# Kernel optimization log

Measured on AMD Instinct MI355X. Metric: run time of the kernel, lower is better.

The kernel has to match this reference:

```python
import jax, jax.numpy as jnp
import numpy as np

# Fixed genome topology (layered DAG, topologically ordered levels)
B = 4096      # batch
N_IN = 512    # input nodes
H1 = 1536     # hidden level 1
H2 = 1536     # hidden level 2
N_OUT = 512   # output nodes
FAN = 32      # fan-in per non-input node


def setup_inputs() -> dict:
    key = jax.random.key(0)
    ks = jax.random.split(key, 10)
    x = jax.random.normal(ks[0], (B, N_IN), dtype=jnp.float32)
    # level 1: sources among inputs [0, N_IN)
    src0 = jax.random.randint(ks[1], (H1 * FAN,), 0, N_IN, dtype=jnp.int32)
    dst0 = jax.random.randint(ks[2], (H1 * FAN,), 0, H1, dtype=jnp.int32)
    w0 = jax.random.normal(ks[3], (H1 * FAN,), dtype=jnp.float32) * 0.1
    # level 2: sources among inputs + level1 [0, N_IN+H1)
    src1 = jax.random.randint(ks[4], (H2 * FAN,), 0, N_IN + H1, dtype=jnp.int32)
    dst1 = jax.random.randint(ks[5], (H2 * FAN,), 0, H2, dtype=jnp.int32)
    w1 = jax.random.normal(ks[6], (H2 * FAN,), dtype=jnp.float32) * 0.1
    # output level: sources among all earlier nodes [0, N_IN+H1+H2)
    src2 = jax.random.randint(ks[7], (N_OUT * FAN,), 0, N_IN + H1 + H2, dtype=jnp.int32)
    dst2 = jax.random.randint(ks[8], (N_OUT * FAN,), 0, N_OUT, dtype=jnp.int32)
    w2 = jax.random.normal(ks[9], (N_OUT * FAN,), dtype=jnp.float32) * 0.1
    return dict(x=x, src0=src0, dst0=dst0, w0=w0,
                src1=src1, dst1=dst1, w1=w1,
                src2=src2, dst2=dst2, w2=w2)


def _level(node_values, src, dst, w, size):
    # per-edge weighted gather: [B, E]
    vals = node_values[:, src] * w
    # scatter-add into destination nodes of this level: [B, size]
    agg = jnp.zeros((node_values.shape[0], size), node_values.dtype).at[:, dst].add(vals)
    # per-node activation (genome.activation == 'relu'); relu(0)=0 matches
    # original's behavior of leaving unconnected nodes at zero
    return jax.nn.relu(agg)


def reference(x, src0, dst0, w0, src1, dst1, w1, src2, dst2, w2):
    nv = x                                        # [B, N_IN]
    h1 = _level(nv, src0, dst0, w0, H1)           # [B, H1]
    nv = jnp.concatenate([nv, h1], axis=1)        # [B, N_IN+H1]
    h2 = _level(nv, src1, dst1, w1, H2)           # [B, H2]
    nv = jnp.concatenate([nv, h2], axis=1)        # [B, N_IN+H1+H2]
    out = _level(nv, src2, dst2, w2, N_OUT)       # [B, N_OUT]
    return out
```

## Files before the change

kernel.cpp:

```cpp
#include <hip/hip_runtime.h>
#include <hip/hip_fp16.h>
#include <stdint.h>

#define BATCH 4096
#define N_IN  512
#define H1    1536
#define H2    1536
#define N_OUT 512
#define FAN   32
#define E0 (H1 * FAN)
#define E1 (H2 * FAN)
#define E2 (N_OUT * FAN)
#define ETOT (E0 + E1 + E2)
#define K1 N_IN
#define K2 (N_IN + H1)
#define K3 (N_IN + H1 + H2)

#define NVSTRIDE 3648
#define NVBYTES  ((size_t)BATCH * NVSTRIDE * 2)
#define W0BYTES  ((size_t)H1 * K1 * 2)
#define W1BYTES  ((size_t)H2 * K2 * 2)
#define W2BYTES  ((size_t)N_OUT * K3 * 2)

typedef _Float16 f16x8 __attribute__((ext_vector_type(8)));
typedef float    f32x4 __attribute__((ext_vector_type(4)));

__global__ __launch_bounds__(256) void k_xcvt(const float* __restrict__ x,
                                              __half* __restrict__ nvT) {
    const int t  = blockIdx.x * 256 + threadIdx.x;
    const int n  = t >> 6;
    const int c8 = t & 63;
    const float4 f0 = *(const float4*)(x + (size_t)n * N_IN + c8 * 8);
    const float4 f1 = *(const float4*)(x + (size_t)n * N_IN + c8 * 8 + 4);
    const __half2 a = __floats2half2_rn(f0.x, f0.y);
    const __half2 b = __floats2half2_rn(f0.z, f0.w);
    const __half2 c = __floats2half2_rn(f1.x, f1.y);
    const __half2 d = __floats2half2_rn(f1.z, f1.w);
    uint4 u;
    u.x = *(const uint32_t*)&a; u.y = *(const uint32_t*)&b;
    u.z = *(const uint32_t*)&c; u.w = *(const uint32_t*)&d;
    *(uint4*)(nvT + (size_t)n * NVSTRIDE + c8 * 8) = u;
}

__device__ __forceinline__ void atomic_add_half(__half* addr, float val) {
    uint32_t* base = (uint32_t*)((size_t)addr & ~(size_t)3);
    const bool hi  = ((size_t)addr & 2) != 0;
    uint32_t old = *base, assumed;
    do {
        assumed = old;
        __half2 h2 = *(__half2*)&assumed;
        float f = (hi ? __high2float(h2) : __low2float(h2)) + val;
        __half2 nh = hi ? __halves2half2(__low2half(h2), __float2half_rn(f))
                        : __halves2half2(__float2half_rn(f), __high2half(h2));
        old = atomicCAS(base, assumed, *(uint32_t*)&nh);
    } while (old != assumed);
}

__global__ __launch_bounds__(256) void k_wfill(const int* __restrict__ src,
                                               const int* __restrict__ dst,
                                               const float* __restrict__ w,
                                               __half* __restrict__ Wd, const int K) {
    const int e = blockIdx.x * 256 + threadIdx.x;
    atomic_add_half(Wd + (size_t)dst[e] * K + src[e], w[e]);
}

__global__ __launch_bounds__(256) void k_wfill_all(
        const int* __restrict__ s0, const int* __restrict__ d0, const float* __restrict__ w0,
        const int* __restrict__ s1, const int* __restrict__ d1, const float* __restrict__ w1,
        const int* __restrict__ s2, const int* __restrict__ d2, const float* __restrict__ w2,
        __half* __restrict__ W0d, __half* __restrict__ W1d, __half* __restrict__ W2d) {
    const int e = blockIdx.x * 256 + threadIdx.x;
    if (e < E0)            atomic_add_half(W0d + (size_t)d0[e] * K1 + s0[e], w0[e]);
    else if (e < E0 + E1) { const int i = e - E0;      atomic_add_half(W1d + (size_t)d1[i] * K2 + s1[i], w1[i]); }
    else                  { const int i = e - E0 - E1; atomic_add_half(W2d + (size_t)d2[i] * K3 + s2[i], w2[i]); }
}

template<int BM, bool F32OUT>
__global__ __launch_bounds__(256, 2)
void k_gemm(const __half* __restrict__ A,
            const __half* __restrict__ Bt,
            __half* __restrict__ Ch,
            float* __restrict__ Cf,
            const int K) {
    constexpr int FM = BM / 32;
    constexpr int WR = BM / 2;
    __shared__ __half lA[2][BM * 64];
    __shared__ __half lB[2][128 * 64];
    const int tid  = threadIdx.x;
    const int lane = tid & 63;
    const int wv   = tid >> 6;
    const int wr   = wv >> 1, wc = wv & 1;
    const int m0   = blockIdx.y * BM;
    const int n0   = blockIdx.x * 128;
    const int lrow = lane >> 3;
    const int lchk = lane & 7;

    f32x4 acc[FM][4] = {};

#define STAGE(BUF, KT) {                                                         \
    _Pragma("unroll")                                                            \
    for (int it = 0; it < BM / 32; ++it) {                                       \
        const int row = it * 32 + wv * 8 + lrow;                                 \
        const int sc  = lchk ^ (row & 7);                                        \
        __builtin_amdgcn_global_load_lds(                                        \
            (const __attribute__((address_space(1))) void*)(const void*)         \
                (A + (size_t)(m0 + row) * K + (KT) + sc * 8),                    \
            (__attribute__((address_space(3))) void*)(void*)                     \
                (lA[BUF] + (it * 32 + wv * 8) * 64),                             \
            16, 0, 0);                                                           \
    }                                                                            \
    _Pragma("unroll")                                                            \
    for (int it = 0; it < 4; ++it) {                                             \
        const int row = it * 32 + wv * 8 + lrow;                                 \
        const int sc  = lchk ^ (row & 7);                                        \
        __builtin_amdgcn_global_load_lds(                                        \
            (const __attribute__((address_space(1))) void*)(const void*)         \
                (Bt + (size_t)(n0 + row) * NVSTRIDE + (KT) + sc * 8),            \
            (__attribute__((address_space(3))) void*)(void*)                     \
                (lB[BUF] + (it * 32 + wv * 8) * 64),                             \
            16, 0, 0);                                                           \
    }                                                                            \
}

    const int NT = K >> 6;
    STAGE(0, 0)
    __syncthreads();

    int cur = 0;
    for (int t = 0; t < NT; ++t) {
        if (t + 1 < NT) STAGE(cur ^ 1, (t + 1) << 6)
#pragma unroll
        for (int kk = 0; kk < 2; ++kk) {
            f16x8 af[FM], bf[4];
#pragma unroll
            for (int fm = 0; fm < FM; ++fm) {
                const int row = wr * WR + fm * 16 + (lane & 15);
                const int ch  = (kk * 4 + (lane >> 4)) ^ (row & 7);
                af[fm] = *(const f16x8*)(lA[cur] + row * 64 + ch * 8);
            }
#pragma unroll
            for (int fn = 0; fn < 4; ++fn) {
                const int row = wc * 64 + fn * 16 + (lane & 15);
                const int ch  = (kk * 4 + (lane >> 4)) ^ (row & 7);
                bf[fn] = *(const f16x8*)(lB[cur] + row * 64 + ch * 8);
            }
#pragma unroll
            for (int fm = 0; fm < FM; ++fm)
#pragma unroll
                for (int fn = 0; fn < 4; ++fn)
                    acc[fm][fn] = __builtin_amdgcn_mfma_f32_16x16x32_f16(
                        af[fm], bf[fn], acc[fm][fn], 0, 0, 0);
        }
        __syncthreads();
        cur ^= 1;
    }
#undef STAGE

    const int cm = (lane >> 4) << 2;
    const int cn = lane & 15;
#pragma unroll
    for (int fm = 0; fm < FM; ++fm) {
#pragma unroll
        for (int fn = 0; fn < 4; ++fn) {
            const f32x4 v = acc[fm][fn];
            const float r0 = fmaxf(v[0], 0.f), r1 = fmaxf(v[1], 0.f);
            const float r2 = fmaxf(v[2], 0.f), r3 = fmaxf(v[3], 0.f);
            const int mm = m0 + wr * WR + fm * 16 + cm;
            const int nn = n0 + wc * 64 + fn * 16 + cn;
            if constexpr (F32OUT) {
                float4 o; o.x = r0; o.y = r1; o.z = r2; o.w = r3;
                *(float4*)(Cf + (size_t)nn * N_OUT + mm) = o;
            } else {
                const __half2 p0 = __floats2half2_rn(r0, r1);
                const __half2 p1 = __floats2half2_rn(r2, r3);
                uint2 u; u.x = *(const uint32_t*)&p0; u.y = *(const uint32_t*)&p1;
                *(uint2*)(Ch + (size_t)nn * NVSTRIDE + mm) = u;
            }
        }
    }
}

extern "C" void kernel_launch(void* const* d_in, const int* in_sizes, int n_in,
                              void* d_out, int out_size, void* d_ws, size_t ws_size,
                              hipStream_t stream) {
    const float* x  = (const float*)d_in[0];
    const int* s0   = (const int*)d_in[1];
    const int* dd0  = (const int*)d_in[2];
    const float* w0 = (const float*)d_in[3];
    const int* s1   = (const int*)d_in[4];
    const int* dd1  = (const int*)d_in[5];
    const float* w1 = (const float*)d_in[6];
    const int* s2   = (const int*)d_in[7];
    const int* dd2  = (const int*)d_in[8];
    const float* w2 = (const float*)d_in[9];

    char*   ws  = (char*)d_ws;
    __half* nvT = (__half*)ws;
    float*  out = (float*)d_out;

    k_xcvt<<<BATCH * 64 / 256, 256, 0, stream>>>(x, nvT);

    if (ws_size >= NVBYTES + W0BYTES + W1BYTES + W2BYTES) {
        __half* W0p = (__half*)(ws + NVBYTES);
        __half* W1p = (__half*)(ws + NVBYTES + W0BYTES);
        __half* W2p = (__half*)(ws + NVBYTES + W0BYTES + W1BYTES);
        hipMemsetAsync(W0p, 0, W0BYTES + W1BYTES + W2BYTES, stream);
        k_wfill_all<<<ETOT / 256, 256, 0, stream>>>(s0, dd0, w0, s1, dd1, w1,
                                                    s2, dd2, w2, W0p, W1p, W2p);
        k_gemm<96, false><<<dim3(BATCH / 128, H1 / 96), 256, 0, stream>>>(
            W0p, nvT, nvT + N_IN, nullptr, K1);
        k_gemm<96, false><<<dim3(BATCH / 128, H2 / 96), 256, 0, stream>>>(
            W1p, nvT, nvT + K2, nullptr, K2);
        k_gemm<64, true><<<dim3(BATCH / 128, N_OUT / 64), 256, 0, stream>>>(
            W2p, nvT, nullptr, out, K3);
    } else {
        __half* Wp = (__half*)(ws + NVBYTES);
        hipMemsetAsync(Wp, 0, W0BYTES, stream);
        k_wfill<<<E0 / 256, 256, 0, stream>>>(s0, dd0, w0, Wp, K1);
        k_gemm<96, false><<<dim3(BATCH / 128, H1 / 96), 256, 0, stream>>>(
            Wp, nvT, nvT + N_IN, nullptr, K1);
        hipMemsetAsync(Wp, 0, W1BYTES, stream);
        k_wfill<<<E1 / 256, 256, 0, stream>>>(s1, dd1, w1, Wp, K2);
        k_gemm<96, false><<<dim3(BATCH / 128, H2 / 96), 256, 0, stream>>>(
            Wp, nvT, nvT + K2, nullptr, K2);
        hipMemsetAsync(Wp, 0, W2BYTES, stream);
        k_wfill<<<E2 / 256, 256, 0, stream>>>(s2, dd2, w2, Wp, K3);
        k_gemm<64, true><<<dim3(BATCH / 128, N_OUT / 64), 256, 0, stream>>>(
            Wp, nvT, nullptr, out, K3);
    }
}
```

Before: 172.0 us.

## Restructure GEMM pipelining, add 3-stage output GEMM, shrink stride, reuse weight buffer

Moves the GEMM K-loop prefetch to an explicit s_waitcnt vmcnt/s_barrier scheme so the next tile's global-to-LDS loads overlap the current tile's MFMAs. Adds a dedicated 512-thread output-layer GEMM with a 4-buffer ring that keeps two tiles in flight. Shrinks the activation row stride from 3648 to 3584, which changes global address alignment. Drops the fallback branch and reuses the layer-0 weight buffer for layer 2, which adds a second memset and fill between GEMMs. The hand-written waitcnt counts must match the number of outstanding loads exactly, or data will be read before it arrives.

After: 161.4 us. 6.2% less time.

```diff
diff --git a/kernel.cpp b/kernel.cpp
--- a/kernel.cpp
+++ b/kernel.cpp
@@ -11,12 +11,11 @@
 #define E0 (H1 * FAN)
 #define E1 (H2 * FAN)
 #define E2 (N_OUT * FAN)
-#define ETOT (E0 + E1 + E2)
 #define K1 N_IN
 #define K2 (N_IN + H1)
 #define K3 (N_IN + H1 + H2)
 
-#define NVSTRIDE 3648
+#define NVSTRIDE 3584
 #define NVBYTES  ((size_t)BATCH * NVSTRIDE * 2)
 #define W0BYTES  ((size_t)H1 * K1 * 2)
 #define W1BYTES  ((size_t)H2 * K2 * 2)
@@ -24,6 +23,11 @@
 
 typedef _Float16 f16x8 __attribute__((ext_vector_type(8)));
 typedef float    f32x4 __attribute__((ext_vector_type(4)));
+
+#define GLL(SRC, DST)                                                        \
+    __builtin_amdgcn_global_load_lds(                                        \
+        (const __attribute__((address_space(1))) void*)(const void*)(SRC),   \
+        (__attribute__((address_space(3))) void*)(void*)(DST), 16, 0, 0)
 
 __global__ __launch_bounds__(256) void k_xcvt(const float* __restrict__ x,
                                               __half* __restrict__ nvT) {
@@ -56,6 +60,15 @@
     } while (old != assumed);
 }
 
+__global__ __launch_bounds__(256) void k_wfill01(
+        const int* __restrict__ s0, const int* __restrict__ d0, const float* __restrict__ w0,
+        const int* __restrict__ s1, const int* __restrict__ d1, const float* __restrict__ w1,
+        __half* __restrict__ W0d, __half* __restrict__ W1d) {
+    const int e = blockIdx.x * 256 + threadIdx.x;
+    if (e < E0)  atomic_add_half(W0d + (size_t)d0[e] * K1 + s0[e], w0[e]);
+    else { const int i = e - E0; atomic_add_half(W1d + (size_t)d1[i] * K2 + s1[i], w1[i]); }
+}
+
 __global__ __launch_bounds__(256) void k_wfill(const int* __restrict__ src,
                                                const int* __restrict__ dst,
                                                const float* __restrict__ w,
@@ -64,77 +77,62 @@
     atomic_add_half(Wd + (size_t)dst[e] * K + src[e], w[e]);
 }
 
-__global__ __launch_bounds__(256) void k_wfill_all(
-        const int* __restrict__ s0, const int* __restrict__ d0, const float* __restrict__ w0,
-        const int* __restrict__ s1, const int* __restrict__ d1, const float* __restrict__ w1,
-        const int* __restrict__ s2, const int* __restrict__ d2, const float* __restrict__ w2,
-        __half* __restrict__ W0d, __half* __restrict__ W1d, __half* __restrict__ W2d) {
-    const int e = blockIdx.x * 256 + threadIdx.x;
-    if (e < E0)            atomic_add_half(W0d + (size_t)d0[e] * K1 + s0[e], w0[e]);
-    else if (e < E0 + E1) { const int i = e - E0;      atomic_add_half(W1d + (size_t)d1[i] * K2 + s1[i], w1[i]); }
-    else                  { const int i = e - E0 - E1; atomic_add_half(W2d + (size_t)d2[i] * K3 + s2[i], w2[i]); }
-}
-
-template<int BM, bool F32OUT>
 __global__ __launch_bounds__(256, 2)
-void k_gemm(const __half* __restrict__ A,
-            const __half* __restrict__ Bt,
-            __half* __restrict__ Ch,
-            float* __restrict__ Cf,
-            const int K) {
-    constexpr int FM = BM / 32;
-    constexpr int WR = BM / 2;
-    __shared__ __half lA[2][BM * 64];
+void k_gemm96(const __half* __restrict__ A,
+              const __half* __restrict__ Bt,
+              __half* __restrict__ Ch,
+              const int K) {
+    __shared__ __half lA[2][96 * 64];
     __shared__ __half lB[2][128 * 64];
     const int tid  = threadIdx.x;
     const int lane = tid & 63;
     const int wv   = tid >> 6;
     const int wr   = wv >> 1, wc = wv & 1;
-    const int m0   = blockIdx.y * BM;
+    const int m0   = blockIdx.y * 96;
     const int n0   = blockIdx.x * 128;
     const int lrow = lane >> 3;
     const int lchk = lane & 7;
 
-    f32x4 acc[FM][4] = {};
-
-#define STAGE(BUF, KT) {                                                         \
-    _Pragma("unroll")                                                            \
-    for (int it = 0; it < BM / 32; ++it) {                                       \
-        const int row = it * 32 + wv * 8 + lrow;                                 \
-        const int sc  = lchk ^ (row & 7);                                        \
-        __builtin_amdgcn_global_load_lds(                                        \
-            (const __attribute__((address_space(1))) void*)(const void*)         \
-                (A + (size_t)(m0 + row) * K + (KT) + sc * 8),                    \
-            (__attribute__((address_space(3))) void*)(void*)                     \
-                (lA[BUF] + (it * 32 + wv * 8) * 64),                             \
-            16, 0, 0);                                                           \
-    }                                                                            \
-    _Pragma("unroll")                                                            \
-    for (int it = 0; it < 4; ++it) {                                             \
-        const int row = it * 32 + wv * 8 + lrow;                                 \
-        const int sc  = lchk ^ (row & 7);                                        \
-        __builtin_amdgcn_global_load_lds(                                        \
-            (const __attribute__((address_space(1))) void*)(const void*)         \
-                (Bt + (size_t)(n0 + row) * NVSTRIDE + (KT) + sc * 8),            \
-            (__attribute__((address_space(3))) void*)(void*)                     \
-                (lB[BUF] + (it * 32 + wv * 8) * 64),                             \
-            16, 0, 0);                                                           \
-    }                                                                            \
+    f32x4 acc[3][4] = {};
+
+#define STAGE96(BUF, KT) {                                                   \
+    _Pragma("unroll")                                                        \
+    for (int it = 0; it < 3; ++it) {                                         \
+        const int row = it * 32 + wv * 8 + lrow;                             \
+        const int sc  = lchk ^ (row & 7);                                    \
+        GLL(A + (size_t)(m0 + row) * K + (KT) + sc * 8,                      \
+            lA[BUF] + (it * 32 + wv * 8) * 64);                              \
+    }                                                                        \
+    _Pragma("unroll")                                                        \
+    for (int it = 0; it < 4; ++it) {                                         \
+        const int row = it * 32 + wv * 8 + lrow;                             \
+        const int sc  = lchk ^ (row & 7);                                    \
+        GLL(Bt + (size_t)(n0 + row) * NVSTRIDE + (KT) + sc * 8,              \
+            lB[BUF] + (it * 32 + wv * 8) * 64);                              \
+    }                                                                        \
 }
 
     const int NT = K >> 6;
-    STAGE(0, 0)
-    __syncthreads();
-
+    STAGE96(0, 0)
     int cur = 0;
     for (int t = 0; t < NT; ++t) {
-        if (t + 1 < NT) STAGE(cur ^ 1, (t + 1) << 6)
+        __builtin_amdgcn_s_barrier();
+        __builtin_amdgcn_sched_barrier(0);
+        if (t + 1 < NT) {
+            STAGE96(cur ^ 1, (t + 1) << 6)
+            asm volatile("s_waitcnt vmcnt(7)" ::: "memory");
+        } else {
+            asm volatile("s_waitcnt vmcnt(0)" ::: "memory");
+        }
+        __builtin_amdgcn_sched_barrier(0);
+        __builtin_amdgcn_s_barrier();
+        __builtin_amdgcn_sched_barrier(0);
 #pragma unroll
         for (int kk = 0; kk < 2; ++kk) {
-            f16x8 af[FM], bf[4];
-#pragma unroll
-            for (int fm = 0; fm < FM; ++fm) {
-                const int row = wr * WR + fm * 16 + (lane & 15);
+            f16x8 af[3], bf[4];
+#pragma unroll
+            for (int fm = 0; fm < 3; ++fm) {
+                const int row = wr * 48 + fm * 16 + (lane & 15);
                 const int ch  = (kk * 4 + (lane >> 4)) ^ (row & 7);
                 af[fm] = *(const f16x8*)(lA[cur] + row * 64 + ch * 8);
             }
@@ -145,39 +143,124 @@
                 bf[fn] = *(const f16x8*)(lB[cur] + row * 64 + ch * 8);
             }
 #pragma unroll
-            for (int fm = 0; fm < FM; ++fm)
+            for (int fm = 0; fm < 3; ++fm)
 #pragma unroll
                 for (int fn = 0; fn < 4; ++fn)
                     acc[fm][fn] = __builtin_amdgcn_mfma_f32_16x16x32_f16(
                         af[fm], bf[fn], acc[fm][fn], 0, 0, 0);
         }
-        __syncthreads();
         cur ^= 1;
     }
-#undef STAGE
+#undef STAGE96
 
     const int cm = (lane >> 4) << 2;
     const int cn = lane & 15;
 #pragma unroll
-    for (int fm = 0; fm < FM; ++fm) {
+    for (int fm = 0; fm < 3; ++fm)
 #pragma unroll
         for (int fn = 0; fn < 4; ++fn) {
             const f32x4 v = acc[fm][fn];
-            const float r0 = fmaxf(v[0], 0.f), r1 = fmaxf(v[1], 0.f);
-            const float r2 = fmaxf(v[2], 0.f), r3 = fmaxf(v[3], 0.f);
-            const int mm = m0 + wr * WR + fm * 16 + cm;
+            const __half2 p0 = __floats2half2_rn(fmaxf(v[0], 0.f), fmaxf(v[1], 0.f));
+            const __half2 p1 = __floats2half2_rn(fmaxf(v[2], 0.f), fmaxf(v[3], 0.f));
+            const int mm = m0 + wr * 48 + fm * 16 + cm;
             const int nn = n0 + wc * 64 + fn * 16 + cn;
-            if constexpr (F32OUT) {
-                float4 o; o.x = r0; o.y = r1; o.z = r2; o.w = r3;
-                *(float4*)(Cf + (size_t)nn * N_OUT + mm) = o;
-            } else {
-                const __half2 p0 = __floats2half2_rn(r0, r1);
-                const __half2 p1 = __floats2half2_rn(r2, r3);
-                uint2 u; u.x = *(const uint32_t*)&p0; u.y = *(const uint32_t*)&p1;
-                *(uint2*)(Ch + (size_t)nn * NVSTRIDE + mm) = u;
-            }
+            uint2 u; u.x = *(const uint32_t*)&p0; u.y = *(const uint32_t*)&p1;
+            *(uint2*)(Ch + (size_t)nn * NVSTRIDE + mm) = u;
+        }
+}
+
+__global__ __launch_bounds__(512, 2)
+void k_gemm3(const __half* __restrict__ A,
+             const __half* __restrict__ Bt,
+             float* __restrict__ Cf) {
+    __shared__ __half lA[4][64 * 64];
+    __shared__ __half lB[4][128 * 64];
+    const int tid  = threadIdx.x;
+    const int lane = tid & 63;
+    const int wv   = tid >> 6;
+    const int wr   = wv >> 2, wc = wv & 3;
+    const int m0   = blockIdx.y * 64;
+    const int n0   = blockIdx.x * 128;
+    const int lrow = lane >> 3;
+    const int lchk = lane & 7;
+    const int K = K3;
+
+    f32x4 acc[2][2] = {};
+
+#define STAGE3(BUF, KT) {                                                    \
+    _Pragma("unroll")                                                        \
+    for (int i = 0; i < 3; ++i) {                                            \
+        const int L = wv * 3 + i;                   \
+        if (L < 8) {                                                         \
+            const int row = L * 8 + lrow;                                    \
+            const int sc  = lchk ^ (row & 7);                                \
+            GLL(A + (size_t)(m0 + row) * K + (KT) + sc * 8,                  \
+                lA[BUF] + L * 512);                                          \
+        } else {                                                             \
+            const int row = (L - 8) * 8 + lrow;                              \
+            const int sc  = lchk ^ (row & 7);                                \
+            GLL(Bt + (size_t)(n0 + row) * NVSTRIDE + (KT) + sc * 8,          \
+                lB[BUF] + (L - 8) * 512);                                    \
+        }                                                                    \
+    }                                                                        \
+}
+
+    const int NT = K >> 6;
+    STAGE3(0, 0)
+    STAGE3(1, 64)
+    for (int t = 0; t < NT; ++t) {
+        if (t + 2 < NT) {
+            STAGE3((t + 2) & 3, (t + 2) << 6)
+            asm volatile("s_waitcnt vmcnt(6)" ::: "memory");
+        } else if (t + 1 < NT) {
+            asm volatile("s_waitcnt vmcnt(3)" ::: "memory");
+        } else {
+            asm volatile("s_waitcnt vmcnt(0)" ::: "memory");
+        }
+        __builtin_amdgcn_sched_barrier(0);
+        __builtin_amdgcn_s_barrier();
+        __builtin_amdgcn_sched_barrier(0);
+        const __half* bA = lA[t & 3];
+        const __half* bB = lB[t & 3];
+#pragma unroll
+        for (int kk = 0; kk < 2; ++kk) {
+            f16x8 af[2], bf[2];
+#pragma unroll
+            for (int fm = 0; fm < 2; ++fm) {
+                const int row = wr * 32 + fm * 16 + (lane & 15);
+                const int ch  = (kk * 4 + (lane >> 4)) ^ (row & 7);
+                af[fm] = *(const f16x8*)(bA + row * 64 + ch * 8);
+            }
+#pragma unroll
+            for (int fn = 0; fn < 2; ++fn) {
+                const int row = wc * 32 + fn * 16 + (lane & 15);
+                const int ch  = (kk * 4 + (lane >> 4)) ^ (row & 7);
+                bf[fn] = *(const f16x8*)(bB + row * 64 + ch * 8);
+            }
+#pragma unroll
+            for (int fm = 0; fm < 2; ++fm)
+#pragma unroll
+                for (int fn = 0; fn < 2; ++fn)
+                    acc[fm][fn] = __builtin_amdgcn_mfma_f32_16x16x32_f16(
+                        af[fm], bf[fn], acc[fm][fn], 0, 0, 0);
         }
     }
+#undef STAGE3
+
+    const int cm = (lane >> 4) << 2;
+    const int cn = lane & 15;
+#pragma unroll
+    for (int fm = 0; fm < 2; ++fm)
+#pragma unroll
+        for (int fn = 0; fn < 2; ++fn) {
+            const f32x4 v = acc[fm][fn];
+            float4 o;
+            o.x = fmaxf(v[0], 0.f); o.y = fmaxf(v[1], 0.f);
+            o.z = fmaxf(v[2], 0.f); o.w = fmaxf(v[3], 0.f);
+            const int mm = m0 + wr * 32 + fm * 16 + cm;
+            const int nn = n0 + wc * 32 + fn * 16 + cn;
+            *(float4*)(Cf + (size_t)nn * N_OUT + mm) = o;
+        }
 }
 
 extern "C" void kernel_launch(void* const* d_in, const int* in_sizes, int n_in,
@@ -196,36 +279,19 @@
 
     char*   ws  = (char*)d_ws;
     __half* nvT = (__half*)ws;
+    __half* W0p = (__half*)(ws + NVBYTES);
+    __half* W1p = (__half*)(ws + NVBYTES + W0BYTES);
+    __half* W2p = W0p;
     float*  out = (float*)d_out;
 
     k_xcvt<<<BATCH * 64 / 256, 256, 0, stream>>>(x, nvT);
 
-    if (ws_size >= NVBYTES + W0BYTES + W1BYTES + W2BYTES) {
-        __half* W0p = (__half*)(ws + NVBYTES);
-        __half* W1p = (__half*)(ws + NVBYTES + W0BYTES);
-        __half* W2p = (__half*)(ws + NVBYTES + W0BYTES + W1BYTES);
-        hipMemsetAsync(W0p, 0, W0BYTES + W1BYTES + W2BYTES, stream);
-        k_wfill_all<<<ETOT / 256, 256, 0, stream>>>(s0, dd0, w0, s1, dd1, w1,
-                                                    s2, dd2, w2, W0p, W1p, W2p);
-        k_gemm<96, false><<<dim3(BATCH / 128, H1 / 96), 256, 0, stream>>>(
-            W0p, nvT, nvT + N_IN, nullptr, K1);
-        k_gemm<96, false><<<dim3(BATCH / 128, H2 / 96), 256, 0, stream>>>(
-            W1p, nvT, nvT + K2, nullptr, K2);
-        k_gemm<64, true><<<dim3(BATCH / 128, N_OUT / 64), 256, 0, stream>>>(
-            W2p, nvT, nullptr, out, K3);
-    } else {
-        __half* Wp = (__half*)(ws + NVBYTES);
-        hipMemsetAsync(Wp, 0, W0BYTES, stream);
-        k_wfill<<<E0 / 256, 256, 0, stream>>>(s0, dd0, w0, Wp, K1);
-        k_gemm<96, false><<<dim3(BATCH / 128, H1 / 96), 256, 0, stream>>>(
-            Wp, nvT, nvT + N_IN, nullptr, K1);
-        hipMemsetAsync(Wp, 0, W1BYTES, stream);
-        k_wfill<<<E1 / 256, 256, 0, stream>>>(s1, dd1, w1, Wp, K2);
-        k_gemm<96, false><<<dim3(BATCH / 128, H2 / 96), 256, 0, stream>>>(
-            Wp, nvT, nvT + K2, nullptr, K2);
-        hipMemsetAsync(Wp, 0, W2BYTES, stream);
-        k_wfill<<<E2 / 256, 256, 0, stream>>>(s2, dd2, w2, Wp, K3);
-        k_gemm<64, true><<<dim3(BATCH / 128, N_OUT / 64), 256, 0, stream>>>(
-            Wp, nvT, nullptr, out, K3);
-    }
-}
+    hipMemsetAsync(W0p, 0, W0BYTES + W1BYTES, stream);
+    k_wfill01<<<(E0 + E1) / 256, 256, 0, stream>>>(s0, dd0, w0, s1, dd1, w1, W0p, W1p);
+    k_gemm96<<<dim3(BATCH / 128, H1 / 96), 256, 0, stream>>>(W0p, nvT, nvT + N_IN, K1);
+    k_gemm96<<<dim3(BATCH / 128, H2 / 96), 256, 0, stream>>>(W1p, nvT, nvT + K2, K2);
+
+    hipMemsetAsync(W2p, 0, W2BYTES, stream);
+    k_wfill<<<E2 / 256, 256, 0, stream>>>(s2, dd2, w2, W2p, K3);
+    k_gemm3<<<dim3(BATCH / 128, N_OUT / 64), 512, 0, stream>>>(W2p, nvT, out);
+}
```
